# Kernel optimization log

Hardware: AMD Instinct MI355X
Metric: run time of the kernel (lower is better)

Reference implementation:

```python
import jax, jax.numpy as jnp
import numpy as np

B, L, N = 32, 512, 512          # batch, seq_len, enc_in (num variables = token dim)
D, H, EL, DF = 512, 8, 2, 2048  # d_model, n_heads (hardcoded 8 in FourierBlock), e_layers, d_ff
PRED, K, MODES = 96, 25, 64     # pred_len, moving_avg kernel, fourier modes (low select)
E = D // H


def setup_inputs() -> dict:
    key = jax.random.key(0)
    ks = jax.random.split(key, 16)
    s = 0.02
    return {
        "x_enc": jax.random.normal(ks[0], (B, L, N), jnp.float32),
        "x_mark_enc": jax.random.normal(ks[1], (B, L, 4), jnp.float32),
        "x_dec": jax.random.normal(ks[2], (B, 144, N), jnp.float32),
        "x_mark_dec": jax.random.normal(ks[3], (B, 144, 4), jnp.float32),
        "W_trend": jax.random.normal(ks[4], (L, PRED), jnp.float32) * s,
        "b_trend": jnp.zeros((PRED,), jnp.float32),
        "W_emb": jax.random.normal(ks[5], (L, D), jnp.float32) * s,
        "b_emb": jnp.zeros((D,), jnp.float32),
        "Wq": jax.random.normal(ks[6], (EL, D, D), jnp.float32) * s,
        "bq": jnp.zeros((EL, D), jnp.float32),
        "Wk": jax.random.normal(ks[7], (EL, D, D), jnp.float32) * s,
        "bk": jnp.zeros((EL, D), jnp.float32),
        "Wv": jax.random.normal(ks[8], (EL, D, D), jnp.float32) * s,
        "bv": jnp.zeros((EL, D), jnp.float32),
        "fw_r": jax.random.uniform(ks[9], (EL, H, E, E, MODES), jnp.float32) / (D * D),
        "fw_i": jax.random.uniform(ks[10], (EL, H, E, E, MODES), jnp.float32) / (D * D),
        "Wo": jax.random.normal(ks[11], (EL, D, D), jnp.float32) * s,
        "bo": jnp.zeros((EL, D), jnp.float32),
        "W1": jax.random.normal(ks[12], (EL, DF, D), jnp.float32) * s,
        "W2": jax.random.normal(ks[13], (EL, D, DF), jnp.float32) * s,
        "ln_g": jnp.ones((D,), jnp.float32),
        "ln_b": jnp.zeros((D,), jnp.float32),
        "W_head": jax.random.normal(ks[14], (D, PRED), jnp.float32) * s,
        "b_head": jnp.zeros((PRED,), jnp.float32),
    }


def series_decomp(x, k):
    # moving average over axis=1 with edge replication padding (Autoformer style)
    pad = (k - 1) // 2
    xp = jnp.concatenate([jnp.repeat(x[:, :1], pad, axis=1), x,
                          jnp.repeat(x[:, -1:], pad, axis=1)], axis=1)
    c = jnp.cumsum(xp, axis=1)
    c = jnp.concatenate([jnp.zeros_like(c[:, :1]), c], axis=1)
    mean = (c[:, k:] - c[:, :-k]) / k
    return x - mean, mean


def fourier_attn(x, Wq, bq, Wk, bk, Wv, bv, fw, Wo, bo):
    # AutoCorrelationLayer wrapping FourierBlock (k/v projections computed but unused)
    b, n, d = x.shape
    q = (x @ Wq + bq).reshape(b, n, H, E)
    _k = (x @ Wk + bk).reshape(b, n, H, E)
    _v = (x @ Wv + bv).reshape(b, n, H, E)
    xq = jnp.transpose(q, (0, 2, 3, 1))        # [B,H,E,N]
    x_ft = jnp.fft.rfft(xq, axis=-1)           # [B,H,E,N//2+1]
    m = fw.shape[-1]
    # low-frequency mode select: index = range(m); out_ft[..., wi] = einsum('bhi,hio->bho')
    out_sel = jnp.einsum('bhim,hiom->bhom', x_ft[..., :m], fw)
    out_ft = jnp.zeros((b, H, E, n // 2 + 1), x_ft.dtype).at[..., :m].set(out_sel)
    xt = jnp.fft.irfft(out_ft, n=n, axis=-1)   # [B,H,E,N]
    out = xt.reshape(b, n, H * E)              # replicates torch .view(B, L, -1) on [B,H,E,L]
    return out @ Wo + bo


def encoder_layer(x, Wq, bq, Wk, bk, Wv, bv, fw, Wo, bo, W1, W2):
    x = x + fourier_attn(x, Wq, bq, Wk, bk, Wv, bv, fw, Wo, bo)
    x, _ = series_decomp(x, K)
    y = jax.nn.gelu(x @ W1.T, approximate=False) @ W2.T  # 1x1 convs, bias=False
    x, _ = series_decomp(x + y, K)
    return x


def my_layernorm(x, g, b):
    mu = jnp.mean(x, -1, keepdims=True)
    var = jnp.var(x, -1, keepdims=True)
    xh = (x - mu) / jnp.sqrt(var + 1e-5) * g + b
    return xh - jnp.mean(xh, axis=1, keepdims=True)  # my_Layernorm: subtract seq-mean


def reference(x_enc, x_mark_enc, x_dec, x_mark_dec, W_trend, b_trend, W_emb, b_emb,
              Wq, bq, Wk, bk, Wv, bv, fw_r, fw_i, Wo, bo, W1, W2, ln_g, ln_b,
              W_head, b_head):
    seasonal, trend = series_decomp(x_enc, K)                         # [B,L,N]
    trend_out = jnp.einsum('bln,lp->bpn', trend, W_trend) + b_trend[None, :, None]
    enc = jnp.einsum('bln,ld->bnd', seasonal, W_emb) + b_emb          # variate tokens [B,N,D]
    for i in range(EL):
        fw = fw_r[i] + 1j * fw_i[i]
        enc = encoder_layer(enc, Wq[i], bq[i], Wk[i], bk[i], Wv[i], bv[i],
                            fw, Wo[i], bo[i], W1[i], W2[i])
    enc = my_layernorm(enc, ln_g, ln_b)
    seasonal_out = jnp.transpose(enc @ W_head + b_head, (0, 2, 1))    # [B,pred,N]
    return seasonal_out + trend_out
```

## Files before the change

kernel.cpp:

```cpp
#include <hip/hip_runtime.h>
#include <math.h>


typedef unsigned short ushort_t;
typedef unsigned int uint_t;
using bf16x8_t = __attribute__((ext_vector_type(8))) short;
using f32x4_t  = __attribute__((ext_vector_type(4))) float;
using u16x8_t  = __attribute__((ext_vector_type(8))) unsigned short;

__device__ __forceinline__ unsigned short f2b(float x) {
    union { float f; uint_t u; } c; c.f = x;
    uint_t r = c.u + 0x7fffu + ((c.u >> 16) & 1u);
    return (unsigned short)(r >> 16);
}
__device__ __forceinline__ float b2f(unsigned short h) {
    union { uint_t u; float f; } c; c.u = ((uint_t)h) << 16; return c.f;
}
__device__ __forceinline__ float gelu_fast(float x) {
    float z = x * (1.5957691216f + 0.0713548163f * x * x);
    return x / (1.f + __expf(-z));
}

#define GCAST(p) ((const __attribute__((address_space(1))) void*)(p))
#define LCAST(p) ((__attribute__((address_space(3))) void*)(p))

enum { ME_F32 = 0, ME_BF16, ME_DCBIAS_BF16, ME_BIASCOL_BF16,
       ME_BIASCOL_ACCB16, ME_GELU_BF16, ME_RESB_BF16, ME_TREND };

template<int EPI>
__global__ __launch_bounds__(512)
void mgemm_k(const ushort_t* __restrict__ A, const ushort_t* __restrict__ B,
             const float* __restrict__ bias, const ushort_t* __restrict__ Resb,
             void* __restrict__ Cv,
             int M, int N, int K, int ldc, int ldres,
             long sA, long sB, long sC, long sRes)
{
    const int gx = gridDim.x, gy = gridDim.y;
    const int nwg = gx * gy * gridDim.z;
    const int lin = (blockIdx.z * gy + blockIdx.y) * gx + blockIdx.x;
    const int cpx = nwg >> 3;
    const int swz = (nwg & 7) ? lin : ((lin & 7) * cpx + (lin >> 3));
    const int bx = swz % gx;
    const int t2 = swz / gx;
    const int by = t2 % gy;
    const int bz = t2 / gy;

    A += bz * sA;
    B += bz * sB;
    const int m0 = by * 128, n0 = bx * 128;

    __shared__ __align__(16) ushort_t As[3][4096];
    __shared__ __align__(16) ushort_t Bs[3][4096];

    const int tid = threadIdx.x;
    const int wave = tid >> 6, lane = tid & 63;
    const int wr = wave >> 1, wc = wave & 1;

    f32x4_t acc[2][4] = {};

    const int srow = tid >> 2;
    const int skof = (tid & 3) * 8;

    const ushort_t* ga = A + (long)(m0 + srow) * K + skof;
    const ushort_t* gb = B + (long)(n0 + srow) * K + skof;
    const int nt = K >> 5;

#define STG(s, bidx) { const long ko = (long)(s) << 5; \
    __builtin_amdgcn_global_load_lds(GCAST(ga + ko), LCAST(As[bidx] + wave * 512), 16, 0, 0); \
    __builtin_amdgcn_global_load_lds(GCAST(gb + ko), LCAST(Bs[bidx] + wave * 512), 16, 0, 0); }

    STG(0, 0)
    STG(1, 1)

    const int kg = (lane >> 4) * 8;
    int cb = 0;

    for (int t = 0; t < nt; ++t) {
        if (t + 1 < nt) { asm volatile("s_waitcnt vmcnt(2)" ::: "memory"); }
        else            { asm volatile("s_waitcnt vmcnt(0)" ::: "memory"); }
        __builtin_amdgcn_s_barrier();
        asm volatile("" ::: "memory");
        __builtin_amdgcn_sched_barrier(0);
        if (t + 2 < nt) { int nb = cb + 2; if (nb >= 3) nb -= 3; STG(t + 2, nb) }

        bf16x8_t a[2], b[4];
        #pragma unroll
        for (int i = 0; i < 2; ++i)
            a[i] = *(const bf16x8_t*)&As[cb][(wr * 32 + i * 16 + (lane & 15)) * 32 + kg];
        #pragma unroll
        for (int j = 0; j < 4; ++j)
            b[j] = *(const bf16x8_t*)&Bs[cb][(wc * 64 + j * 16 + (lane & 15)) * 32 + kg];
        #pragma unroll
        for (int i = 0; i < 2; ++i)
            #pragma unroll
            for (int j = 0; j < 4; ++j)
                acc[i][j] = __builtin_amdgcn_mfma_f32_16x16x32_bf16(a[i], b[j], acc[i][j], 0, 0, 0);
        ++cb; if (cb >= 3) cb = 0;
    }
#undef STG

    float*    Cf  = (float*)Cv + bz * sC;
    ushort_t* Cb  = (ushort_t*)Cv + bz * sC;
    const ushort_t* R = Resb ? Resb + bz * sRes : nullptr;

    #pragma unroll
    for (int i = 0; i < 2; ++i) {
        #pragma unroll
        for (int j = 0; j < 4; ++j) {
            #pragma unroll
            for (int r = 0; r < 4; ++r) {
                int gm = m0 + wr * 32 + i * 16 + (lane >> 4) * 4 + r;
                int gn = n0 + wc * 64 + j * 16 + (lane & 15);
                float v = acc[i][j][r];
                long idx = (long)gm * ldc + gn;
                if (EPI == ME_F32)               Cf[idx] = v;
                else if (EPI == ME_BF16)         Cb[idx] = f2b(v);
                else if (EPI == ME_BIASCOL_BF16) Cb[idx] = f2b(v + bias[gn]);
                else if (EPI == ME_BIASCOL_ACCB16) Cb[idx] = f2b(b2f(Cb[idx]) + v + bias[gn]);
                else if (EPI == ME_GELU_BF16)    Cb[idx] = f2b(gelu_fast(v));
                else if (EPI == ME_RESB_BF16)    Cb[idx] = f2b(v + b2f(R[(long)gm * ldres + gn]));
            }
        }
    }
}

template<int EPI>
__global__ __launch_bounds__(256)
void sgemm_k(const ushort_t* __restrict__ A, const ushort_t* __restrict__ B,
             const float* __restrict__ bias, void* __restrict__ Cv,
             int M, int N, int K, int ldc,
             long sA, long sB, long sC)
{
    const int gx = gridDim.x, gy = gridDim.y;
    const int nwg = gx * gy * gridDim.z;
    const int lin = (blockIdx.z * gy + blockIdx.y) * gx + blockIdx.x;
    const int cpx = nwg >> 3;
    const int swz = (nwg & 7) ? lin : ((lin & 7) * cpx + (lin >> 3));
    const int bx = swz % gx;
    const int t2 = swz / gx;
    const int by = t2 % gy;
    const int bz = t2 / gy;

    A += bz * sA;
    B += bz * sB;
    const int m0 = by * 64, n0 = bx * 64;

    __shared__ __align__(16) ushort_t As[3][2048];
    __shared__ __align__(16) ushort_t Bs[3][2048];

    const int tid = threadIdx.x;
    const int wave = tid >> 6, lane = tid & 63;
    const int wr = wave >> 1, wc = wave & 1;

    f32x4_t acc[2][2] = {};

    const int srow = tid >> 2;
    const int skof = (tid & 3) * 8;

    const ushort_t* ga = A + (long)(m0 + srow) * K + skof;
    const ushort_t* gb = B + (long)(n0 + srow) * K + skof;
    const int nt = K >> 5;

#define STG(s, bidx) { const long ko = (long)(s) << 5; \
    __builtin_amdgcn_global_load_lds(GCAST(ga + ko), LCAST(As[bidx] + wave * 512), 16, 0, 0); \
    __builtin_amdgcn_global_load_lds(GCAST(gb + ko), LCAST(Bs[bidx] + wave * 512), 16, 0, 0); }

    STG(0, 0)
    STG(1, 1)

    const int kg = (lane >> 4) * 8;
    int cb = 0;

    for (int t = 0; t < nt; ++t) {
        if (t + 1 < nt) { asm volatile("s_waitcnt vmcnt(2)" ::: "memory"); }
        else            { asm volatile("s_waitcnt vmcnt(0)" ::: "memory"); }
        __builtin_amdgcn_s_barrier();
        asm volatile("" ::: "memory");
        __builtin_amdgcn_sched_barrier(0);
        if (t + 2 < nt) { int nb = cb + 2; if (nb >= 3) nb -= 3; STG(t + 2, nb) }

        bf16x8_t a[2], b[2];
        #pragma unroll
        for (int i = 0; i < 2; ++i)
            a[i] = *(const bf16x8_t*)&As[cb][(wr * 32 + i * 16 + (lane & 15)) * 32 + kg];
        #pragma unroll
        for (int j = 0; j < 2; ++j)
            b[j] = *(const bf16x8_t*)&Bs[cb][(wc * 32 + j * 16 + (lane & 15)) * 32 + kg];
        #pragma unroll
        for (int i = 0; i < 2; ++i)
            #pragma unroll
            for (int j = 0; j < 2; ++j)
                acc[i][j] = __builtin_amdgcn_mfma_f32_16x16x32_bf16(a[i], b[j], acc[i][j], 0, 0, 0);
        ++cb; if (cb >= 3) cb = 0;
    }
#undef STG

    float*    Cf = (float*)Cv + bz * sC;
    ushort_t* Cb = (ushort_t*)Cv + bz * sC;

    #pragma unroll
    for (int i = 0; i < 2; ++i) {
        #pragma unroll
        for (int j = 0; j < 2; ++j) {
            #pragma unroll
            for (int r = 0; r < 4; ++r) {
                int gm = m0 + wr * 32 + i * 16 + (lane >> 4) * 4 + r;
                int gn = n0 + wc * 32 + j * 16 + (lane & 15);
                float v = acc[i][j][r];
                long idx = (long)gm * ldc + gn;
                if (EPI == ME_F32)               Cf[idx] = v;
                else if (EPI == ME_BF16)         Cb[idx] = f2b(v);
                else if (EPI == ME_DCBIAS_BF16)  Cb[idx] = f2b(v + (gn == 0 ? 512.f * bias[gm] : 0.f));
                else if (EPI == ME_TREND) { if (gm < 96) Cf[idx] = v + bias[gm]; }
            }
        }
    }
}

__global__ __launch_bounds__(256)
void fmix_k(const ushort_t* __restrict__ A2, const ushort_t* __restrict__ B2,
            ushort_t* __restrict__ OS)
{
    const int hm = blockIdx.x;
    const int h = hm >> 6, m = hm & 63;
    __shared__ __align__(16) ushort_t As[32 * 128];
    __shared__ __align__(16) ushort_t Bs[128 * 128];

    const int tid = threadIdx.x;
    const int w = tid >> 6, lane = tid & 63;

    const ushort_t* Ag = A2 + (long)hm * 4096;
    const ushort_t* Bg = B2 + (long)hm * 16384;
    #pragma unroll
    for (int r = 0; r < 2; ++r)
        __builtin_amdgcn_global_load_lds(GCAST(Ag + w * 1024 + r * 512 + lane * 8),
                                         LCAST(As + w * 1024 + r * 512), 16, 0, 0);
    #pragma unroll
    for (int r = 0; r < 8; ++r)
        __builtin_amdgcn_global_load_lds(GCAST(Bg + w * 4096 + r * 512 + lane * 8),
                                         LCAST(Bs + w * 4096 + r * 512), 16, 0, 0);
    __syncthreads();

    f32x4_t acc[2][2] = {};
    const int kg = (lane >> 4) * 8;
    #pragma unroll
    for (int kk = 0; kk < 4; ++kk) {
        bf16x8_t a[2], b[2];
        #pragma unroll
        for (int i = 0; i < 2; ++i)
            a[i] = *(const bf16x8_t*)&As[(i * 16 + (lane & 15)) * 128 + kk * 32 + kg];
        #pragma unroll
        for (int j = 0; j < 2; ++j)
            b[j] = *(const bf16x8_t*)&Bs[(w * 32 + j * 16 + (lane & 15)) * 128 + kk * 32 + kg];
        #pragma unroll
        for (int i = 0; i < 2; ++i)
            #pragma unroll
            for (int j = 0; j < 2; ++j)
                acc[i][j] = __builtin_amdgcn_mfma_f32_16x16x32_bf16(a[i], b[j], acc[i][j], 0, 0, 0);
    }

    #pragma unroll
    for (int i = 0; i < 2; ++i) {
        #pragma unroll
        for (int j = 0; j < 2; ++j) {
            #pragma unroll
            for (int r = 0; r < 4; ++r) {
                int b = i * 16 + (lane >> 4) * 4 + r;
                int n2 = w * 32 + j * 16 + (lane & 15);
                int o = n2 & 63, ri = n2 >> 6;
                OS[((long)b * 512 + h * 64 + o) * 128 + ri * 64 + m] = f2b(acc[i][j][r]);
            }
        }
    }
}

__global__ __launch_bounds__(256)
void bprep_k(const float* __restrict__ FR, const float* __restrict__ FI,
             ushort_t* __restrict__ B2)
{
    const int bx = blockIdx.x;
    const int h = bx >> 6, o = bx & 63;
    __shared__ float fr_s[64][65];
    __shared__ float fi_s[64][65];
    for (int e = threadIdx.x; e < 4096; e += 256) {
        int i = e >> 6, m = e & 63;
        long src = ((long)(h * 64 + i) * 64 + o) * 64 + m;
        fr_s[i][m] = FR[src];
        fi_s[i][m] = FI[src];
    }
    __syncthreads();
    const int m = threadIdx.x & 63;
    const int kq = threadIdx.x >> 6;
    ushort_t* b0 = B2 + ((long)(h * 64 + m) * 128 + o) * 128;
    ushort_t* b1 = B2 + ((long)(h * 64 + m) * 128 + o + 64) * 128;
    for (int kk = 0; kk < 32; ++kk) {
        int k2 = kq * 32 + kk;
        int ik = k2 & 63, hi = k2 >> 6;
        float fr = fr_s[ik][m], fi = fi_s[ik][m];
        b0[k2] = f2b(hi ? -fi : fr);
        b1[k2] = f2b(hi ?  fr : fi);
    }
}

__global__ __launch_bounds__(256)
void aprep_k(const ushort_t* __restrict__ XFTb, ushort_t* __restrict__ A2)
{
    const int bx = blockIdx.x;
    const int b = bx >> 3, h = bx & 7;
    __shared__ ushort_t xs[64][130];
    for (int e = threadIdx.x; e < 8192; e += 256) {
        int i = e >> 7, mp = e & 127;
        xs[i][mp] = XFTb[((long)b * 512 + h * 64 + i) * 128 + mp];
    }
    __syncthreads();
    const int m = threadIdx.x & 63;
    const int kq = threadIdx.x >> 6;
    ushort_t* dst = A2 + ((long)(h * 64 + m) * 32 + b) * 128;
    for (int kk = 0; kk < 32; ++kk) {
        int k2 = kq * 32 + kk;
        int i = k2 & 63, ri = k2 >> 6;
        dst[k2] = xs[i][ri * 64 + m];
    }
}

__global__ __launch_bounds__(256)
void decomp2_k(const float* __restrict__ X, ushort_t* __restrict__ Sb,
               ushort_t* __restrict__ Trb)
{
    const int id = blockIdx.x;
    const int ch = id & 1, rc = (id >> 1) & 31, b = id >> 6;
    const int c = ch * 256 + threadIdx.x;
    const int r0 = rc * 16;
    const long base = ((long)b << 18) + c;
    float s = 0.f;
    #pragma unroll
    for (int j = -12; j <= 12; ++j) {
        int rr = r0 + j; rr = rr < 0 ? 0 : (rr > 511 ? 511 : rr);
        s += X[base + ((long)rr << 9)];
    }
    for (int rr = 0; rr < 16; ++rr) {
        int r = r0 + rr;
        float mean = s * (1.f / 25.f);
        long idx = base + ((long)r << 9);
        float x = X[idx];
        if (Sb)  Sb[idx] = f2b(x - mean);
        if (Trb) Trb[idx] = f2b(mean);
        int rp = r + 13; rp = rp > 511 ? 511 : rp;
        int rm = r - 12; rm = rm < 0 ? 0 : rm;
        s += X[base + ((long)rp << 9)] - X[base + ((long)rm << 9)];
    }
}

__global__ __launch_bounds__(256)
void decomp2v_k(const ushort_t* __restrict__ Xb, ushort_t* __restrict__ Sb)
{
    const int id = blockIdx.x;
    const int b = id >> 4, rc = id & 15;
    const int c0 = (threadIdx.x & 63) * 8;
    const int rsub = threadIdx.x >> 6;
    const int r0 = rc * 32 + rsub * 8;
    const ushort_t* base = Xb + ((long)b << 18) + c0;
    ushort_t* obase = Sb + ((long)b << 18) + c0;

    float s[8] = {};
    #pragma unroll
    for (int j = -12; j <= 12; ++j) {
        int rr = r0 + j; rr = rr < 0 ? 0 : (rr > 511 ? 511 : rr);
        u16x8_t v = *(const u16x8_t*)(base + ((long)rr << 9));
        #pragma unroll
        for (int k = 0; k < 8; ++k) s[k] += b2f(v[k]);
    }
    for (int rr = 0; rr < 8; ++rr) {
        int r = r0 + rr;
        u16x8_t xv = *(const u16x8_t*)(base + ((long)r << 9));
        u16x8_t ov;
        #pragma unroll
        for (int k = 0; k < 8; ++k) ov[k] = f2b(b2f(xv[k]) - s[k] * (1.f / 25.f));
        *(u16x8_t*)(obase + ((long)r << 9)) = ov;
        int rp = r + 13; rp = rp > 511 ? 511 : rp;
        int rm = r - 12; rm = rm < 0 ? 0 : rm;
        u16x8_t vp = *(const u16x8_t*)(base + ((long)rp << 9));
        u16x8_t vm = *(const u16x8_t*)(base + ((long)rm << 9));
        #pragma unroll
        for (int k = 0; k < 8; ++k) s[k] += b2f(vp[k]) - b2f(vm[k]);
    }
}

__global__ __launch_bounds__(256)
void init_tables_k(ushort_t* __restrict__ TFb, ushort_t* __restrict__ TI2b)
{
    int t = blockIdx.x * 256 + threadIdx.x;
    const float w = 6.283185307179586f / 512.f;
    if (t < 65536) {
        int mp = t >> 9, n = t & 511;
        int m = mp & 63;
        float ang = ((m * n) & 511) * w;
        TFb[t] = f2b((mp < 64) ? cosf(ang) : -sinf(ang));
    } else {
        int u = t - 65536;
        int mp = u >> 9, n = u & 511;
        int m = mp & 63;
        float ang = ((m * n) & 511) * w;
        float v;
        if (mp < 64) v = (m == 0) ? (1.f / 512.f) : (2.f / 512.f) * cosf(ang);
        else         v = (m == 0) ? 0.f : -(2.f / 512.f) * sinf(ang);
        TI2b[u] = f2b(v);
    }
}

__global__ __launch_bounds__(256)
void f2b_k(const float* __restrict__ X, ushort_t* __restrict__ Y, long n)
{
    long i = ((long)blockIdx.x * 256 + threadIdx.x) * 8;
    if (i >= n) return;
    const float4* xp = (const float4*)(X + i);
    float4 v0 = xp[0], v1 = xp[1];
    u16x8_t o;
    o[0] = f2b(v0.x); o[1] = f2b(v0.y); o[2] = f2b(v0.z); o[3] = f2b(v0.w);
    o[4] = f2b(v1.x); o[5] = f2b(v1.y); o[6] = f2b(v1.z); o[7] = f2b(v1.w);
    *(u16x8_t*)(Y + i) = o;
}

__global__ __launch_bounds__(256)
void trans_b_k(const float* __restrict__ X, ushort_t* __restrict__ Y,
               int R, int C, long sX, long sY)
{
    __shared__ float t[32][33];
    X += (long)blockIdx.z * sX;
    Y += (long)blockIdx.z * sY;
    int r0 = blockIdx.y * 32, c0 = blockIdx.x * 32;
    int tx = threadIdx.x & 31, ty = threadIdx.x >> 5;
    #pragma unroll
    for (int i = ty; i < 32; i += 8)
        t[i][tx] = X[(long)(r0 + i) * C + c0 + tx];
    __syncthreads();
    #pragma unroll
    for (int i = ty; i < 32; i += 8)
        Y[(long)(c0 + i) * R + r0 + tx] = f2b(t[tx][i]);
}

__global__ __launch_bounds__(256)
void trans_bb_k(const ushort_t* __restrict__ X, ushort_t* __restrict__ Y,
                int R, int C, long sX, long sY)
{
    __shared__ ushort_t t[32][34];
    X += (long)blockIdx.z * sX;
    Y += (long)blockIdx.z * sY;
    int r0 = blockIdx.y * 32, c0 = blockIdx.x * 32;
    int tx = threadIdx.x & 31, ty = threadIdx.x >> 5;
    #pragma unroll
    for (int i = ty; i < 32; i += 8)
        t[i][tx] = X[(long)(r0 + i) * C + c0 + tx];
    __syncthreads();
    #pragma unroll
    for (int i = ty; i < 32; i += 8)
        Y[(long)(c0 + i) * R + r0 + tx] = t[tx][i];
}

__global__ __launch_bounds__(256)
void ln_rows_bb_k(const ushort_t* __restrict__ Xb, const float* __restrict__ g,
                  const float* __restrict__ bta, ushort_t* __restrict__ Yb)
{
    int wave = threadIdx.x >> 6, lane = threadIdx.x & 63;
    long row = (long)blockIdx.x * 4 + wave;
    const ushort_t* x = Xb + row * 512 + lane * 8;
    u16x8_t v = *(const u16x8_t*)x;
    float f[8];
    float s = 0.f, ss = 0.f;
    #pragma unroll
    for (int j = 0; j < 8; ++j) { f[j] = b2f(v[j]); s += f[j]; ss += f[j] * f[j]; }
    #pragma unroll
    for (int o = 32; o; o >>= 1) { s += __shfl_xor(s, o); ss += __shfl_xor(ss, o); }
    float mu = s * (1.f / 512.f);
    float var = ss * (1.f / 512.f) - mu * mu;
    float inv = rsqrtf(var + 1e-5f);
    u16x8_t ov;
    #pragma unroll
    for (int j = 0; j < 8; ++j)
        ov[j] = f2b((f[j] - mu) * inv * g[lane * 8 + j] + bta[lane * 8 + j]);
    *(u16x8_t*)(Yb + row * 512 + lane * 8) = ov;
}

__global__ __launch_bounds__(256)
void colmean_bb_k(const ushort_t* __restrict__ Y, ushort_t* __restrict__ O)
{
    __shared__ float ps[4][64];
    int b = blockIdx.x, dg = blockIdx.y;
    int wave = threadIdx.x >> 6, lane = threadIdx.x & 63;
    int d = dg * 64 + lane;
    long base = (long)b * 262144 + d;
    float s = 0.f;
    for (int t = wave * 128; t < wave * 128 + 128; ++t)
        s += b2f(Y[base + ((long)t << 9)]);
    ps[wave][lane] = s;
    __syncthreads();
    float mean = (ps[0][lane] + ps[1][lane] + ps[2][lane] + ps[3][lane]) * (1.f / 512.f);
    for (int t = wave * 128; t < wave * 128 + 128; ++t)
        O[base + ((long)t << 9)] = f2b(b2f(Y[base + ((long)t << 9)]) - mean);
}

__global__ __launch_bounds__(256)
void headadd_k(const float* __restrict__ Th, const float* __restrict__ bh,
               float* __restrict__ out)
{
    const int id = blockIdx.x;
    const int b = id >> 4, t0 = (id & 15) * 32;
    __shared__ float tile[32][100];
    for (int e = threadIdx.x; e < 32 * 96; e += 256) {
        int tl = e / 96, p = e - tl * 96;
        tile[tl][p] = Th[((long)(b * 512 + t0 + tl)) * 128 + p];
    }
    __syncthreads();
    for (int e = threadIdx.x; e < 96 * 32; e += 256) {
        int p = e >> 5, tl = e & 31;
        out[(long)b * 49152 + p * 512 + t0 + tl] += tile[tl][p] + bh[p];
    }
}

extern "C" void kernel_launch(void* const* d_in, const int* in_sizes, int n_in,
                              void* d_out, int out_size, void* d_ws, size_t ws_size,
                              hipStream_t stream)
{
    const float* x_enc   = (const float*)d_in[0];
    const float* W_trend = (const float*)d_in[4];
    const float* b_trend = (const float*)d_in[5];
    const float* W_emb   = (const float*)d_in[6];
    const float* b_emb   = (const float*)d_in[7];
    const float* Wq      = (const float*)d_in[8];
    const float* bq      = (const float*)d_in[9];
    const float* fw_r    = (const float*)d_in[14];
    const float* fw_i    = (const float*)d_in[15];
    const float* Wo      = (const float*)d_in[16];
    const float* bo      = (const float*)d_in[17];
    const float* W1      = (const float*)d_in[18];
    const float* W2      = (const float*)d_in[19];
    const float* ln_g    = (const float*)d_in[20];
    const float* ln_b    = (const float*)d_in[21];
    const float* W_head  = (const float*)d_in[22];
    const float* b_head  = (const float*)d_in[23];
    float* out = (float*)d_out;
    float* ws  = (float*)d_ws;

    const long F = 8388608;
    float* G    = ws;
    ushort_t* xw  = (ushort_t*)(ws + 3 * F);
    ushort_t* xs  = (ushort_t*)(ws + 4 * F);
    ushort_t* T1b = xs + 8388608;
    ushort_t* qT  = (ushort_t*)(ws + 5 * F);

    ushort_t* trendb = (ushort_t*)G;
    ushort_t* seasb  = (ushort_t*)(G + 4194304);
    ushort_t* XFTb  = (ushort_t*)G;
    ushort_t* Yb    = (ushort_t*)(G + 1048576);
    ushort_t* A2    = (ushort_t*)(G + 2097152);
    ushort_t* OSELb = (ushort_t*)(G + 3145728);
    ushort_t* xbT   = (ushort_t*)(G + 4194304);
    ushort_t* B2    = (ushort_t*)(G + 8388608);
    float*    Thead = G;
    ushort_t* gb    = (ushort_t*)G;

    ushort_t* WembT  = (ushort_t*)(ws + 6 * F);
    ushort_t* WTq2   = WembT + 262144;
    ushort_t* WTo2   = WTq2 + 524288;
    ushort_t* W1b2   = WTo2 + 524288;
    ushort_t* W2b2   = W1b2 + 2097152;
    ushort_t* TFb    = W2b2 + 2097152;
    ushort_t* TI2b   = TFb + 65536;
    ushort_t* WtT    = TI2b + 65536;
    ushort_t* WheadT = WtT + 65536;
    ushort_t* TIWob2 = WheadT + 65536;

    dim3 blk(256), blk5(512);

    init_tables_k<<<dim3(512), blk, 0, stream>>>(TFb, TI2b);

    decomp2_k<<<dim3(2048), blk, 0, stream>>>(x_enc, seasb, trendb);

    trans_b_k<<<dim3(3, 16, 1), blk, 0, stream>>>(W_trend, WtT, 512, 96, 0L, 0L);
    trans_b_k<<<dim3(3, 16, 1), blk, 0, stream>>>(W_head, WheadT, 512, 96, 0L, 0L);
    trans_b_k<<<dim3(16, 16, 1), blk, 0, stream>>>(W_emb, WembT, 512, 512, 0L, 0L);
    trans_b_k<<<dim3(16, 16, 2), blk, 0, stream>>>(Wq, WTq2, 512, 512, 262144L, 262144L);
    trans_b_k<<<dim3(16, 16, 2), blk, 0, stream>>>(Wo, WTo2, 512, 512, 262144L, 262144L);
    f2b_k<<<dim3(1024), blk, 0, stream>>>(W1, W1b2, 2097152L);
    f2b_k<<<dim3(1024), blk, 0, stream>>>(W2, W2b2, 2097152L);
    sgemm_k<ME_BF16><<<dim3(2, 8, 2), blk, 0, stream>>>(
        WTo2, TI2b, nullptr, TIWob2,
        512, 128, 512, 128, 262144L, 0L, 65536L);

    trans_bb_k<<<dim3(16, 16, 32), blk, 0, stream>>>(trendb, qT, 512, 512, 262144L, 262144L);
    sgemm_k<ME_TREND><<<dim3(8, 2, 32), blk, 0, stream>>>(
        WtT, qT, b_trend, out,
        128, 512, 512, 512, 0L, 262144L, 49152L);

    trans_bb_k<<<dim3(16, 16, 32), blk, 0, stream>>>(seasb, qT, 512, 512, 262144L, 262144L);
    mgemm_k<ME_BIASCOL_BF16><<<dim3(4, 4, 32), blk5, 0, stream>>>(
        qT, WembT, b_emb, nullptr, xw,
        512, 512, 512, 512, 0, 262144L, 0L, 262144L, 0L);

    for (int l = 0; l < 2; ++l) {
        const float* bq_l = bq + (long)l * 512;
        const float* bo_l = bo + (long)l * 512;
        const float* fr_l = fw_r + (long)l * 2097152;
        const float* fi_l = fw_i + (long)l * 2097152;
        const ushort_t* WTq_l   = WTq2 + (long)l * 262144;
        const ushort_t* W1b_l   = W1b2 + (long)l * 1048576;
        const ushort_t* W2b_l   = W2b2 + (long)l * 1048576;
        const ushort_t* TIWob_l = TIWob2 + (long)l * 65536;

        bprep_k<<<dim3(512), blk, 0, stream>>>(fr_l, fi_l, B2);

        trans_bb_k<<<dim3(16, 16, 32), blk, 0, stream>>>(xw, xbT, 512, 512, 262144L, 262144L);

        sgemm_k<ME_BF16><<<dim3(8, 2, 32), blk, 0, stream>>>(
            TFb, xbT, nullptr, Yb,
            128, 512, 512, 512, 0L, 262144L, 65536L);

        sgemm_k<ME_DCBIAS_BF16><<<dim3(2, 8, 32), blk, 0, stream>>>(
            WTq_l, Yb, bq_l, XFTb,
            512, 128, 512, 128, 0L, 65536L, 65536L);

        aprep_k<<<dim3(256), blk, 0, stream>>>(XFTb, A2);
        fmix_k<<<dim3(512), blk, 0, stream>>>(A2, B2, OSELb);

        mgemm_k<ME_BIASCOL_ACCB16><<<dim3(4, 128, 1), blk5, 0, stream>>>(
            OSELb, TIWob_l, bo_l, nullptr, xw,
            16384, 512, 128, 512, 0, 0L, 0L, 0L, 0L);

        decomp2v_k<<<dim3(512), blk, 0, stream>>>(xw, xs);

        mgemm_k<ME_GELU_BF16><<<dim3(16, 128, 1), blk5, 0, stream>>>(
            xs, W1b_l, nullptr, nullptr, gb,
            16384, 2048, 512, 2048, 0, 0L, 0L, 0L, 0L);
        mgemm_k<ME_RESB_BF16><<<dim3(4, 128, 1), blk5, 0, stream>>>(
            gb, W2b_l, nullptr, xs, T1b,
            16384, 512, 2048, 512, 512, 0L, 0L, 0L, 0L);

        decomp2v_k<<<dim3(512), blk, 0, stream>>>(T1b, xw);
    }

    ln_rows_bb_k<<<dim3(4096), blk, 0, stream>>>(xw, ln_g, ln_b, T1b);
    colmean_bb_k<<<dim3(32, 8), blk, 0, stream>>>(T1b, xs);

    sgemm_k<ME_F32><<<dim3(2, 256, 1), blk, 0, stream>>>(
        xs, WheadT, nullptr, Thead,
        16384, 128, 512, 128, 0L, 0L, 0L);

    headadd_k<<<dim3(512), blk, 0, stream>>>(Thead, b_head, out);
}
```

Measured before the change: 564.9 us.

## Swizzle LDS tiles in GEMMs and write decomposition outputs pre-transposed

Applies an XOR swizzle to the shared-memory layout of the GEMM and Fourier-mix tiles. Global loads write to permuted LDS positions and the fragment reads use the matching permutation, to reduce LDS bank conflicts. Separately, the series-decomposition kernel now writes the seasonal and trend outputs already transposed, as vectorized 8-element stores, which removes two full batch transpose launches. The risk is getting the swizzle index arithmetic exactly consistent between the writer and reader sides.

```diff
diff --git a/kernel.cpp b/kernel.cpp
--- a/kernel.cpp
+++ b/kernel.cpp
@@ -59,7 +59,7 @@
     f32x4_t acc[2][4] = {};
 
     const int srow = tid >> 2;
-    const int skof = (tid & 3) * 8;
+    const int skof = (((tid & 3) ^ ((tid >> 2) & 3)) << 3);
 
     const ushort_t* ga = A + (long)(m0 + srow) * K + skof;
     const ushort_t* gb = B + (long)(n0 + srow) * K + skof;
@@ -72,8 +72,8 @@
     STG(0, 0)
     STG(1, 1)
 
-    const int kg = (lane >> 4) * 8;
-    int cb = 0;
+    const int q = lane >> 4;
+    int cbuf = 0;
 
     for (int t = 0; t < nt; ++t) {
         if (t + 1 < nt) { asm volatile("s_waitcnt vmcnt(2)" ::: "memory"); }
@@ -81,21 +81,25 @@
         __builtin_amdgcn_s_barrier();
         asm volatile("" ::: "memory");
         __builtin_amdgcn_sched_barrier(0);
-        if (t + 2 < nt) { int nb = cb + 2; if (nb >= 3) nb -= 3; STG(t + 2, nb) }
+        if (t + 2 < nt) { int nb = cbuf + 2; if (nb >= 3) nb -= 3; STG(t + 2, nb) }
 
         bf16x8_t a[2], b[4];
         #pragma unroll
-        for (int i = 0; i < 2; ++i)
-            a[i] = *(const bf16x8_t*)&As[cb][(wr * 32 + i * 16 + (lane & 15)) * 32 + kg];
-        #pragma unroll
-        for (int j = 0; j < 4; ++j)
-            b[j] = *(const bf16x8_t*)&Bs[cb][(wc * 64 + j * 16 + (lane & 15)) * 32 + kg];
+        for (int i = 0; i < 2; ++i) {
+            int ra = wr * 32 + i * 16 + (lane & 15);
+            a[i] = *(const bf16x8_t*)&As[cbuf][ra * 32 + ((q ^ (ra & 3)) << 3)];
+        }
+        #pragma unroll
+        for (int j = 0; j < 4; ++j) {
+            int rb = wc * 64 + j * 16 + (lane & 15);
+            b[j] = *(const bf16x8_t*)&Bs[cbuf][rb * 32 + ((q ^ (rb & 3)) << 3)];
+        }
         #pragma unroll
         for (int i = 0; i < 2; ++i)
             #pragma unroll
             for (int j = 0; j < 4; ++j)
                 acc[i][j] = __builtin_amdgcn_mfma_f32_16x16x32_bf16(a[i], b[j], acc[i][j], 0, 0, 0);
-        ++cb; if (cb >= 3) cb = 0;
+        ++cbuf; if (cbuf >= 3) cbuf = 0;
     }
 #undef STG
 
@@ -155,7 +159,7 @@
     f32x4_t acc[2][2] = {};
 
     const int srow = tid >> 2;
-    const int skof = (tid & 3) * 8;
+    const int skof = (((tid & 3) ^ ((tid >> 2) & 3)) << 3);
 
     const ushort_t* ga = A + (long)(m0 + srow) * K + skof;
     const ushort_t* gb = B + (long)(n0 + srow) * K + skof;
@@ -168,8 +172,8 @@
     STG(0, 0)
     STG(1, 1)
 
-    const int kg = (lane >> 4) * 8;
-    int cb = 0;
+    const int q = lane >> 4;
+    int cbuf = 0;
 
     for (int t = 0; t < nt; ++t) {
         if (t + 1 < nt) { asm volatile("s_waitcnt vmcnt(2)" ::: "memory"); }
@@ -177,21 +181,25 @@
         __builtin_amdgcn_s_barrier();
         asm volatile("" ::: "memory");
         __builtin_amdgcn_sched_barrier(0);
-        if (t + 2 < nt) { int nb = cb + 2; if (nb >= 3) nb -= 3; STG(t + 2, nb) }
+        if (t + 2 < nt) { int nb = cbuf + 2; if (nb >= 3) nb -= 3; STG(t + 2, nb) }
 
         bf16x8_t a[2], b[2];
         #pragma unroll
-        for (int i = 0; i < 2; ++i)
-            a[i] = *(const bf16x8_t*)&As[cb][(wr * 32 + i * 16 + (lane & 15)) * 32 + kg];
-        #pragma unroll
-        for (int j = 0; j < 2; ++j)
-            b[j] = *(const bf16x8_t*)&Bs[cb][(wc * 32 + j * 16 + (lane & 15)) * 32 + kg];
+        for (int i = 0; i < 2; ++i) {
+            int ra = wr * 32 + i * 16 + (lane & 15);
+            a[i] = *(const bf16x8_t*)&As[cbuf][ra * 32 + ((q ^ (ra & 3)) << 3)];
+        }
+        #pragma unroll
+        for (int j = 0; j < 2; ++j) {
+            int rb = wc * 32 + j * 16 + (lane & 15);
+            b[j] = *(const bf16x8_t*)&Bs[cbuf][rb * 32 + ((q ^ (rb & 3)) << 3)];
+        }
         #pragma unroll
         for (int i = 0; i < 2; ++i)
             #pragma unroll
             for (int j = 0; j < 2; ++j)
                 acc[i][j] = __builtin_amdgcn_mfma_f32_16x16x32_bf16(a[i], b[j], acc[i][j], 0, 0, 0);
-        ++cb; if (cb >= 3) cb = 0;
+        ++cbuf; if (cbuf >= 3) cbuf = 0;
     }
 #undef STG
 
@@ -232,26 +240,34 @@
     const ushort_t* Ag = A2 + (long)hm * 4096;
     const ushort_t* Bg = B2 + (long)hm * 16384;
     #pragma unroll
-    for (int r = 0; r < 2; ++r)
-        __builtin_amdgcn_global_load_lds(GCAST(Ag + w * 1024 + r * 512 + lane * 8),
-                                         LCAST(As + w * 1024 + r * 512), 16, 0, 0);
-    #pragma unroll
-    for (int r = 0; r < 8; ++r)
-        __builtin_amdgcn_global_load_lds(GCAST(Bg + w * 4096 + r * 512 + lane * 8),
-                                         LCAST(Bs + w * 4096 + r * 512), 16, 0, 0);
+    for (int r = 0; r < 2; ++r) {
+        int rowA = w * 8 + r * 4 + (lane >> 4);
+        const ushort_t* src = Ag + rowA * 128 + (((lane & 15) ^ (rowA & 15)) << 3);
+        __builtin_amdgcn_global_load_lds(GCAST(src), LCAST(As + w * 1024 + r * 512), 16, 0, 0);
+    }
+    #pragma unroll
+    for (int r = 0; r < 8; ++r) {
+        int rowB = w * 32 + r * 4 + (lane >> 4);
+        const ushort_t* src = Bg + rowB * 128 + (((lane & 15) ^ (rowB & 15)) << 3);
+        __builtin_amdgcn_global_load_lds(GCAST(src), LCAST(Bs + w * 4096 + r * 512), 16, 0, 0);
+    }
     __syncthreads();
 
     f32x4_t acc[2][2] = {};
-    const int kg = (lane >> 4) * 8;
     #pragma unroll
     for (int kk = 0; kk < 4; ++kk) {
+        const int cq = kk * 4 + (lane >> 4);
         bf16x8_t a[2], b[2];
         #pragma unroll
-        for (int i = 0; i < 2; ++i)
-            a[i] = *(const bf16x8_t*)&As[(i * 16 + (lane & 15)) * 128 + kk * 32 + kg];
-        #pragma unroll
-        for (int j = 0; j < 2; ++j)
-            b[j] = *(const bf16x8_t*)&Bs[(w * 32 + j * 16 + (lane & 15)) * 128 + kk * 32 + kg];
+        for (int i = 0; i < 2; ++i) {
+            int ra = i * 16 + (lane & 15);
+            a[i] = *(const bf16x8_t*)&As[ra * 128 + ((cq ^ (ra & 15)) << 3)];
+        }
+        #pragma unroll
+        for (int j = 0; j < 2; ++j) {
+            int rb = w * 32 + j * 16 + (lane & 15);
+            b[j] = *(const bf16x8_t*)&Bs[rb * 128 + ((cq ^ (rb & 15)) << 3)];
+        }
         #pragma unroll
         for (int i = 0; i < 2; ++i)
             #pragma unroll
@@ -324,8 +340,8 @@
 }
 
 __global__ __launch_bounds__(256)
-void decomp2_k(const float* __restrict__ X, ushort_t* __restrict__ Sb,
-               ushort_t* __restrict__ Trb)
+void decomp2t_k(const float* __restrict__ X, ushort_t* __restrict__ SbT,
+                ushort_t* __restrict__ TrbT)
 {
     const int id = blockIdx.x;
     const int ch = id & 1, rc = (id >> 1) & 31, b = id >> 6;
@@ -338,17 +354,20 @@
         int rr = r0 + j; rr = rr < 0 ? 0 : (rr > 511 ? 511 : rr);
         s += X[base + ((long)rr << 9)];
     }
+    u16x8_t sv0, sv1, tv0, tv1;
     for (int rr = 0; rr < 16; ++rr) {
         int r = r0 + rr;
         float mean = s * (1.f / 25.f);
-        long idx = base + ((long)r << 9);
-        float x = X[idx];
-        if (Sb)  Sb[idx] = f2b(x - mean);
-        if (Trb) Trb[idx] = f2b(mean);
+        float x = X[base + ((long)r << 9)];
+        if (rr < 8) { sv0[rr] = f2b(x - mean); tv0[rr] = f2b(mean); }
+        else        { sv1[rr - 8] = f2b(x - mean); tv1[rr - 8] = f2b(mean); }
         int rp = r + 13; rp = rp > 511 ? 511 : rp;
         int rm = r - 12; rm = rm < 0 ? 0 : rm;
         s += X[base + ((long)rp << 9)] - X[base + ((long)rm << 9)];
     }
+    long obase = (long)b * 262144 + (long)c * 512 + r0;
+    *(u16x8_t*)&SbT[obase] = sv0;  *(u16x8_t*)&SbT[obase + 8] = sv1;
+    *(u16x8_t*)&TrbT[obase] = tv0; *(u16x8_t*)&TrbT[obase + 8] = tv1;
 }
 
 __global__ __launch_bounds__(256)
@@ -548,8 +567,7 @@
     ushort_t* T1b = xs + 8388608;
     ushort_t* qT  = (ushort_t*)(ws + 5 * F);
 
-    ushort_t* trendb = (ushort_t*)G;
-    ushort_t* seasb  = (ushort_t*)(G + 4194304);
+    ushort_t* trendT = (ushort_t*)G;
     ushort_t* XFTb  = (ushort_t*)G;
     ushort_t* Yb    = (ushort_t*)(G + 1048576);
     ushort_t* A2    = (ushort_t*)(G + 2097152);
@@ -574,7 +592,7 @@
 
     init_tables_k<<<dim3(512), blk, 0, stream>>>(TFb, TI2b);
 
-    decomp2_k<<<dim3(2048), blk, 0, stream>>>(x_enc, seasb, trendb);
+    decomp2t_k<<<dim3(2048), blk, 0, stream>>>(x_enc, qT, trendT);
 
     trans_b_k<<<dim3(3, 16, 1), blk, 0, stream>>>(W_trend, WtT, 512, 96, 0L, 0L);
     trans_b_k<<<dim3(3, 16, 1), blk, 0, stream>>>(W_head, WheadT, 512, 96, 0L, 0L);
@@ -587,12 +605,10 @@
         WTo2, TI2b, nullptr, TIWob2,
         512, 128, 512, 128, 262144L, 0L, 65536L);
 
-    trans_bb_k<<<dim3(16, 16, 32), blk, 0, stream>>>(trendb, qT, 512, 512, 262144L, 262144L);
     sgemm_k<ME_TREND><<<dim3(8, 2, 32), blk, 0, stream>>>(
-        WtT, qT, b_trend, out,
+        WtT, trendT, b_trend, out,
         128, 512, 512, 512, 0L, 262144L, 49152L);
 
-    trans_bb_k<<<dim3(16, 16, 32), blk, 0, stream>>>(seasb, qT, 512, 512, 262144L, 262144L);
     mgemm_k<ME_BIASCOL_BF16><<<dim3(4, 4, 32), blk5, 0, stream>>>(
         qT, WembT, b_emb, nullptr, xw,
         512, 512, 512, 512, 0, 262144L, 0L, 262144L, 0L);
```

Measured after the change: 546.1 us. 3.3% less time.
